# Kernel tuning notes

Hardware: AMD Instinct MI355X
Metric: run time of the kernel (lower is better)

Reference implementation:

```python
import jax, jax.numpy as jnp
import numpy as np

B, S, HID, NH = 4, 2048, 1024, 16
HD = HID // NH  # head_dim = 64


def setup_inputs() -> dict:
    key = jax.random.key(0)
    ks = jax.random.split(key, 5)
    scale = 0.02
    return {
        "hidden_states": jax.random.normal(ks[0], (B, S, HID), dtype=jnp.float32),
        "attention_mask": jnp.zeros((B, 1, 1, S), dtype=jnp.float32),
        "Wq": jax.random.normal(ks[1], (HID, HID), dtype=jnp.float32) * scale,
        "bq": jnp.zeros((HID,), dtype=jnp.float32),
        "Wk": jax.random.normal(ks[2], (HID, HID), dtype=jnp.float32) * scale,
        "bk": jnp.zeros((HID,), dtype=jnp.float32),
        "Wv": jax.random.normal(ks[3], (HID, HID), dtype=jnp.float32) * scale,
        "bv": jnp.zeros((HID,), dtype=jnp.float32),
    }


def _split_heads(x):
    # [B, S, HID] -> [B, NH, S, HD]
    b, s, _ = x.shape
    return x.reshape(b, s, NH, HD).transpose(0, 2, 1, 3)


def reference(hidden_states, attention_mask, Wq, bq, Wk, bk, Wv, bv):
    # Linear projections (torch Linear: x @ W.T + b)
    q = _split_heads(hidden_states @ Wq.T + bq)
    k = _split_heads(hidden_states @ Wk.T + bk)
    v = _split_heads(hidden_states @ Wv.T + bv)

    # scores: [B, NH, S, S]
    scores = jnp.einsum("bhqd,bhkd->bhqk", q, k) / jnp.sqrt(jnp.float32(HD))
    scores = scores + attention_mask  # additive mask, broadcast over heads/query
    weights = jax.nn.softmax(scores, axis=-1)
    # dropout prob = 0 (inference), head_mask = None

    context = jnp.einsum("bhqk,bhkd->bhqd", weights, v)
    # [B, NH, S, HD] -> [B, S, HID]
    context = context.transpose(0, 2, 1, 3).reshape(hidden_states.shape[0], hidden_states.shape[1], HID)
    return context
```

## Files before the change

kernel.cpp:

```cpp
#include <hip/hip_runtime.h>
#include <stdint.h>


typedef float f32x4 __attribute__((ext_vector_type(4)));
typedef float f32x16 __attribute__((ext_vector_type(16)));
typedef __bf16 bf16x8 __attribute__((ext_vector_type(8)));
typedef unsigned short ushort_t;

#define MFMA16(a, b, c) __builtin_amdgcn_mfma_f32_16x16x32_bf16(a, b, c, 0, 0, 0)
#define MFMA32(a, b, c) __builtin_amdgcn_mfma_f32_32x32x16_bf16(a, b, c, 0, 0, 0)

__device__ __forceinline__ ushort_t f2b(float f) {
    union { float f; uint32_t u; } x{f};
    uint32_t r = (x.u + 0x7fffu + ((x.u >> 16) & 1u)) >> 16;
    return (ushort_t)r;
}

__device__ __forceinline__ void gld_lds16(const void* g, void* l) {
    __builtin_amdgcn_global_load_lds(
        (const __attribute__((address_space(1))) unsigned int*)g,
        (__attribute__((address_space(3))) unsigned int*)l, 16, 0, 0);
}

__global__ __launch_bounds__(256) void convert_k(
    const float* __restrict__ hs, const float* __restrict__ wq,
    const float* __restrict__ wk, const float* __restrict__ wv,
    ushort_t* __restrict__ hs_b, ushort_t* __restrict__ w_b) {
    size_t c = (size_t)blockIdx.x * 256 + threadIdx.x;
    size_t i = c * 8;
    const size_t NHS = (size_t)8192 * 1024;
    const float* src;
    ushort_t* dst;
    if (i < NHS) { src = hs + i; dst = hs_b + i; }
    else {
        size_t j = i - NHS;
        int w = (int)(j >> 20);
        size_t o = j & ((1u << 20) - 1);
        src = (w == 0 ? wq : (w == 1 ? wk : wv)) + o;
        dst = w_b + ((size_t)w << 20) + o;
    }
    float4 a = *(const float4*)src;
    float4 b = *(const float4*)(src + 4);
    uint32_t p0 = (uint32_t)f2b(a.x) | ((uint32_t)f2b(a.y) << 16);
    uint32_t p1 = (uint32_t)f2b(a.z) | ((uint32_t)f2b(a.w) << 16);
    uint32_t p2 = (uint32_t)f2b(b.x) | ((uint32_t)f2b(b.y) << 16);
    uint32_t p3 = (uint32_t)f2b(b.z) | ((uint32_t)f2b(b.w) << 16);
    uint4 v{p0, p1, p2, p3};
    *(uint4*)dst = v;
}

__global__ __launch_bounds__(256, 2) void qkv_gemm(
    const ushort_t* __restrict__ Ab, const ushort_t* __restrict__ Wb,
    const float* __restrict__ bq, const float* __restrict__ bk,
    const float* __restrict__ bv, ushort_t* __restrict__ q_ws,
    ushort_t* __restrict__ k_ws, ushort_t* __restrict__ vt_ws) {
    __shared__ __align__(16) char smem_raw[128 * 136 * 2];
    ushort_t* At = (ushort_t*)smem_raw;
    ushort_t* Bt = At + 128 * 64;
    ushort_t* Ct = (ushort_t*)smem_raw;
    int which = blockIdx.z;
    const ushort_t* W = Wb + ((size_t)which << 20);
    int m0 = blockIdx.y * 128, n0 = blockIdx.x * 128;
    int t = threadIdx.x, lane = t & 63, wave = t >> 6;
    int quad = lane >> 4, l16 = lane & 15;
    int wr = (wave >> 1) * 64, wc = (wave & 1) * 64;
    f32x4 acc[4][4] = {};
    for (int k0 = 0; k0 < 1024; k0 += 64) {
        for (int r = 0; r < 4; r++) {
            int idx = r * 256 + t;
            int row = idx >> 3, co = (idx & 7) * 8;
            gld_lds16(Ab + (size_t)(m0 + row) * 1024 + k0 + co, At + idx * 8);
            gld_lds16(W + (size_t)(n0 + row) * 1024 + k0 + co, Bt + idx * 8);
        }
        asm volatile("s_waitcnt vmcnt(0)" ::: "memory");
        __syncthreads();
        for (int kk = 0; kk < 2; kk++) {
            bf16x8 af[4], bf[4];
            for (int i = 0; i < 4; i++)
                af[i] = *(const bf16x8*)(At + (wr + i * 16 + l16) * 64 + kk * 32 + quad * 8);
            for (int j = 0; j < 4; j++)
                bf[j] = *(const bf16x8*)(Bt + (wc + j * 16 + l16) * 64 + kk * 32 + quad * 8);
            for (int i = 0; i < 4; i++)
                for (int j = 0; j < 4; j++)
                    acc[i][j] = MFMA16(af[i], bf[j], acc[i][j]);
        }
        __syncthreads();
    }
    const float* bias = which == 0 ? bq : (which == 1 ? bk : bv);
    float sc = which == 0 ? 0.125f : 1.0f;
    if (which == 2) {
        for (int j = 0; j < 4; j++) {
            float bias_v = bias[n0 + wc + j * 16 + l16];
            for (int i = 0; i < 4; i++) {
                ushort4 pk;
                pk.x = f2b(acc[i][j].x + bias_v);
                pk.y = f2b(acc[i][j].y + bias_v);
                pk.z = f2b(acc[i][j].z + bias_v);
                pk.w = f2b(acc[i][j].w + bias_v);
                *(ushort4*)(Ct + (wc + j * 16 + l16) * 136 + wr + i * 16 + quad * 4) = pk;
            }
        }
    } else {
        for (int j = 0; j < 4; j++) {
            float bias_v = bias[n0 + wc + j * 16 + l16];
            int col = wc + j * 16 + l16;
            for (int i = 0; i < 4; i++) {
                int rb = wr + i * 16 + quad * 4;
                Ct[(rb + 0) * 136 + col] = f2b((acc[i][j].x + bias_v) * sc);
                Ct[(rb + 1) * 136 + col] = f2b((acc[i][j].y + bias_v) * sc);
                Ct[(rb + 2) * 136 + col] = f2b((acc[i][j].z + bias_v) * sc);
                Ct[(rb + 3) * 136 + col] = f2b((acc[i][j].w + bias_v) * sc);
            }
        }
    }
    __syncthreads();
    for (int r = 0; r < 8; r++) {
        int idx = r * 256 + t;
        int row = idx >> 4, c8 = (idx & 15) * 8;
        uint4 val = *(const uint4*)(Ct + row * 136 + c8);
        if (which == 2) {
            int col = n0 + row, h = col >> 6, d = col & 63;
            int tok = m0 + c8, b = tok >> 11, s = tok & 2047;
            *(uint4*)(vt_ws + ((size_t)(b * 16 + h) * 64 + d) * 2048 + s) = val;
        } else {
            int tok = m0 + row, b = tok >> 11, s = tok & 2047;
            int col = n0 + c8, h = col >> 6, d = col & 63;
            ushort_t* base = which == 0 ? q_ws : k_ws;
            *(uint4*)(base + ((size_t)(b * 16 + h) * 2048 + s) * 64 + d) = val;
        }
    }
}

__global__ __launch_bounds__(256, 4) void attn_k(
    const ushort_t* __restrict__ q_ws, const ushort_t* __restrict__ k_ws,
    const ushort_t* __restrict__ vt_ws, const float* __restrict__ mask,
    float* __restrict__ out) {
    __shared__ __align__(16) ushort_t Kl[64 * 72];
    __shared__ __align__(16) ushort_t Vtl[64 * 72];
    __shared__ __align__(16) ushort_t Pl[4][32 * 72];
    int bh = blockIdx.y, b = bh >> 4, h = bh & 15;
    int q0 = blockIdx.x * 128;
    int t = threadIdx.x, lane = t & 63, w = t >> 6;
    int l31 = lane & 31, hi = lane >> 5;
    const ushort_t* Q = q_ws + (size_t)bh * 2048 * 64;
    const ushort_t* K = k_ws + (size_t)bh * 2048 * 64;
    const ushort_t* Vt = vt_ws + (size_t)bh * 64 * 2048;
    const float* mrow = mask + b * 2048;

    bf16x8 qf[4];
#pragma unroll
    for (int c = 0; c < 4; c++)
        qf[c] = *(const bf16x8*)(Q + (size_t)(q0 + w * 32 + l31) * 64 + c * 16 + hi * 8);
    f32x16 o0 = {}, o1 = {};
    float rsum[16];
#pragma unroll
    for (int r = 0; r < 16; r++) rsum[r] = 0.f;

    for (int t0 = 0; t0 < 2048; t0 += 64) {
#pragma unroll
        for (int r = 0; r < 2; r++) {
            int idx = r * 256 + t;
            int row = idx >> 3, co = (idx & 7) * 8;
            *(uint4*)(Kl + row * 72 + co) = *(const uint4*)(K + (size_t)(t0 + row) * 64 + co);
            *(uint4*)(Vtl + row * 72 + co) = *(const uint4*)(Vt + (size_t)row * 2048 + t0 + co);
        }
        float mk0 = mrow[t0 + l31];
        float mk1 = mrow[t0 + 32 + l31];
        __syncthreads();
        f32x16 s0 = {}, s1 = {};
#pragma unroll
        for (int c = 0; c < 4; c++) {
            bf16x8 k0 = *(const bf16x8*)(Kl + l31 * 72 + c * 16 + hi * 8);
            bf16x8 k1 = *(const bf16x8*)(Kl + (32 + l31) * 72 + c * 16 + hi * 8);
            s0 = MFMA32(qf[c], k0, s0);
            s1 = MFMA32(qf[c], k1, s1);
        }
        ushort_t* Pw = Pl[w];
#pragma unroll
        for (int r = 0; r < 16; r++) {
            int prow = (r & 3) + 8 * (r >> 2) + 4 * hi;
            float p0 = __expf(s0[r] + mk0);
            float p1 = __expf(s1[r] + mk1);
            rsum[r] += p0 + p1;
            Pw[prow * 72 + l31] = f2b(p0);
            Pw[prow * 72 + 32 + l31] = f2b(p1);
        }
        asm volatile("s_waitcnt lgkmcnt(0)" ::: "memory");
#pragma unroll
        for (int c = 0; c < 4; c++) {
            bf16x8 pf = *(const bf16x8*)(Pw + l31 * 72 + c * 16 + hi * 8);
            bf16x8 v0 = *(const bf16x8*)(Vtl + l31 * 72 + c * 16 + hi * 8);
            bf16x8 v1 = *(const bf16x8*)(Vtl + (32 + l31) * 72 + c * 16 + hi * 8);
            o0 = MFMA32(pf, v0, o0);
            o1 = MFMA32(pf, v1, o1);
        }
        __syncthreads();
    }
#pragma unroll
    for (int m = 1; m < 32; m <<= 1)
#pragma unroll
        for (int r = 0; r < 16; r++)
            rsum[r] += __shfl_xor(rsum[r], m, 64);
#pragma unroll
    for (int r = 0; r < 16; r++) {
        float inv = 1.f / rsum[r];
        int srow = q0 + w * 32 + (r & 3) + 8 * (r >> 2) + 4 * hi;
        size_t rb = ((size_t)(b * 2048 + srow)) * 1024 + h * 64;
        out[rb + l31] = o0[r] * inv;
        out[rb + 32 + l31] = o1[r] * inv;
    }
}

extern "C" void kernel_launch(void* const* d_in, const int* in_sizes, int n_in,
                              void* d_out, int out_size, void* d_ws, size_t ws_size,
                              hipStream_t stream) {
    const float* hs = (const float*)d_in[0];
    const float* mask = (const float*)d_in[1];
    const float* wq = (const float*)d_in[2];
    const float* bq = (const float*)d_in[3];
    const float* wk = (const float*)d_in[4];
    const float* bk = (const float*)d_in[5];
    const float* wv = (const float*)d_in[6];
    const float* bv = (const float*)d_in[7];
    float* out = (float*)d_out;
    char* ws = (char*)d_ws;
    ushort_t* hs_b = (ushort_t*)ws;
    ushort_t* w_b = (ushort_t*)(ws + 16777216);
    ushort_t* q_ws = (ushort_t*)(ws + 23068672);
    ushort_t* k_ws = (ushort_t*)(ws + 39845888);
    ushort_t* vt_ws = (ushort_t*)(ws + 56623104);

    convert_k<<<5632, 256, 0, stream>>>(hs, wq, wk, wv, hs_b, w_b);
    qkv_gemm<<<dim3(8, 64, 3), 256, 0, stream>>>(hs_b, w_b, bq, bk, bv, q_ws, k_ws, vt_ws);
    attn_k<<<dim3(16, 64), 256, 0, stream>>>(q_ws, k_ws, vt_ws, mask, out);
}
```

Before: 284.1 us.

## Transpose attention MFMAs to keep P in registers, swizzle LDS, use exp2

Rewrites the attention kernel to compute S^T = K·Q^T, so each lane holds probabilities for a single query row. P is then repacked into bf16 fragments with lane shuffles, removing the LDS round trip for P. K and V^T tiles are loaded with direct global-to-LDS loads into an XOR-swizzled layout without padding. Softmax switches to exp2 with log2(e) folded into the Q scale and a pre-scaled mask held in LDS, and the row sum becomes a single scalar per lane. Output goes through an LDS transpose so global stores are coalesced. This adds shuffle and permute work and uses truncating bf16 packing instead of round-to-nearest.

Measured after the change: 266.2 us. 6.3% less time.

```diff
diff --git a/kernel.cpp b/kernel.cpp
--- a/kernel.cpp
+++ b/kernel.cpp
@@ -6,6 +6,7 @@
 typedef float f32x16 __attribute__((ext_vector_type(16)));
 typedef __bf16 bf16x8 __attribute__((ext_vector_type(8)));
 typedef unsigned short ushort_t;
+typedef uint32_t u32;
 
 #define MFMA16(a, b, c) __builtin_amdgcn_mfma_f32_16x16x32_bf16(a, b, c, 0, 0, 0)
 #define MFMA32(a, b, c) __builtin_amdgcn_mfma_f32_32x32x16_bf16(a, b, c, 0, 0, 0)
@@ -14,6 +15,25 @@
     union { float f; uint32_t u; } x{f};
     uint32_t r = (x.u + 0x7fffu + ((x.u >> 16) & 1u)) >> 16;
     return (ushort_t)r;
+}
+
+__device__ __forceinline__ float fexp2(float x) {
+#if __has_builtin(__builtin_amdgcn_exp2f)
+    return __builtin_amdgcn_exp2f(x);
+#else
+    return exp2f(x);
+#endif
+}
+
+__device__ __forceinline__ u32 pkpair(float e, float o) {
+    union { float f; u32 u; } xe{e}, xo{o};
+    return __builtin_amdgcn_perm(xo.u, xe.u, 0x07060302u);
+}
+
+__device__ __forceinline__ bf16x8 mk8(u32 a, u32 b, u32 c, u32 d) {
+    union { u32 u[4]; bf16x8 v; } x;
+    x.u[0] = a; x.u[1] = b; x.u[2] = c; x.u[3] = d;
+    return x.v;
 }
 
 __device__ __forceinline__ void gld_lds16(const void* g, void* l) {
@@ -87,7 +107,7 @@
         __syncthreads();
     }
     const float* bias = which == 0 ? bq : (which == 1 ? bk : bv);
-    float sc = which == 0 ? 0.125f : 1.0f;
+    float sc = which == 0 ? (0.125f * 1.44269504f) : 1.0f;
     if (which == 2) {
         for (int j = 0; j < 4; j++) {
             float bias_v = bias[n0 + wc + j * 16 + l16];
@@ -135,79 +155,118 @@
     const ushort_t* __restrict__ q_ws, const ushort_t* __restrict__ k_ws,
     const ushort_t* __restrict__ vt_ws, const float* __restrict__ mask,
     float* __restrict__ out) {
-    __shared__ __align__(16) ushort_t Kl[64 * 72];
-    __shared__ __align__(16) ushort_t Vtl[64 * 72];
-    __shared__ __align__(16) ushort_t Pl[4][32 * 72];
+    __shared__ __align__(16) char smraw[128 * 65 * 4];
+    ushort_t* Kl = (ushort_t*)smraw;
+    ushort_t* Vtl = Kl + 64 * 64;
+    float* Ml2 = (float*)(smraw + 16384);
+    float* Ot = (float*)smraw;
+
     int bh = blockIdx.y, b = bh >> 4, h = bh & 15;
     int q0 = blockIdx.x * 128;
     int t = threadIdx.x, lane = t & 63, w = t >> 6;
     int l31 = lane & 31, hi = lane >> 5;
+    bool h0 = (hi == 0);
     const ushort_t* Q = q_ws + (size_t)bh * 2048 * 64;
     const ushort_t* K = k_ws + (size_t)bh * 2048 * 64;
     const ushort_t* Vt = vt_ws + (size_t)bh * 64 * 2048;
-    const float* mrow = mask + b * 2048;
-
+
+    for (int r = 0; r < 8; r++) {
+        int i = r * 256 + t;
+        Ml2[i] = mask[b * 2048 + i] * 1.44269504f;
+    }
     bf16x8 qf[4];
 #pragma unroll
-    for (int c = 0; c < 4; c++)
-        qf[c] = *(const bf16x8*)(Q + (size_t)(q0 + w * 32 + l31) * 64 + c * 16 + hi * 8);
+    for (int cs = 0; cs < 4; cs++)
+        qf[cs] = *(const bf16x8*)(Q + (size_t)(q0 + w * 32 + l31) * 64 + cs * 16 + hi * 8);
+    int co[4];
+#pragma unroll
+    for (int cs = 0; cs < 4; cs++)
+        co[cs] = ((cs * 2 + hi) ^ (l31 & 7)) * 8;
+
     f32x16 o0 = {}, o1 = {};
-    float rsum[16];
-#pragma unroll
-    for (int r = 0; r < 16; r++) rsum[r] = 0.f;
+    float rs = 0.f;
 
     for (int t0 = 0; t0 < 2048; t0 += 64) {
 #pragma unroll
-        for (int r = 0; r < 2; r++) {
-            int idx = r * 256 + t;
-            int row = idx >> 3, co = (idx & 7) * 8;
-            *(uint4*)(Kl + row * 72 + co) = *(const uint4*)(K + (size_t)(t0 + row) * 64 + co);
-            *(uint4*)(Vtl + row * 72 + co) = *(const uint4*)(Vt + (size_t)row * 2048 + t0 + co);
-        }
-        float mk0 = mrow[t0 + l31];
-        float mk1 = mrow[t0 + 32 + l31];
+        for (int it = 0; it < 2; it++) {
+            int idx = it * 256 + t;
+            int row = idx >> 3, ch = idx & 7;
+            int sch = (ch ^ (row & 7)) * 8;
+            gld_lds16(K + (size_t)(t0 + row) * 64 + sch, Kl + idx * 8);
+            gld_lds16(Vt + (size_t)row * 2048 + t0 + sch, Vtl + idx * 8);
+        }
+        asm volatile("s_waitcnt vmcnt(0)" ::: "memory");
         __syncthreads();
         f32x16 s0 = {}, s1 = {};
 #pragma unroll
-        for (int c = 0; c < 4; c++) {
-            bf16x8 k0 = *(const bf16x8*)(Kl + l31 * 72 + c * 16 + hi * 8);
-            bf16x8 k1 = *(const bf16x8*)(Kl + (32 + l31) * 72 + c * 16 + hi * 8);
-            s0 = MFMA32(qf[c], k0, s0);
-            s1 = MFMA32(qf[c], k1, s1);
-        }
-        ushort_t* Pw = Pl[w];
-#pragma unroll
-        for (int r = 0; r < 16; r++) {
-            int prow = (r & 3) + 8 * (r >> 2) + 4 * hi;
-            float p0 = __expf(s0[r] + mk0);
-            float p1 = __expf(s1[r] + mk1);
-            rsum[r] += p0 + p1;
-            Pw[prow * 72 + l31] = f2b(p0);
-            Pw[prow * 72 + 32 + l31] = f2b(p1);
-        }
-        asm volatile("s_waitcnt lgkmcnt(0)" ::: "memory");
-#pragma unroll
-        for (int c = 0; c < 4; c++) {
-            bf16x8 pf = *(const bf16x8*)(Pw + l31 * 72 + c * 16 + hi * 8);
-            bf16x8 v0 = *(const bf16x8*)(Vtl + l31 * 72 + c * 16 + hi * 8);
-            bf16x8 v1 = *(const bf16x8*)(Vtl + (32 + l31) * 72 + c * 16 + hi * 8);
-            o0 = MFMA32(pf, v0, o0);
-            o1 = MFMA32(pf, v1, o1);
-        }
-        __syncthreads();
-    }
-#pragma unroll
-    for (int m = 1; m < 32; m <<= 1)
-#pragma unroll
-        for (int r = 0; r < 16; r++)
-            rsum[r] += __shfl_xor(rsum[r], m, 64);
+        for (int cs = 0; cs < 4; cs++) {
+            bf16x8 k0 = *(const bf16x8*)(Kl + l31 * 64 + co[cs]);
+            bf16x8 k1 = *(const bf16x8*)(Kl + (32 + l31) * 64 + co[cs]);
+            s0 = MFMA32(k0, qf[cs], s0);
+            s1 = MFMA32(k1, qf[cs], s1);
+        }
+        u32 pa[8], pb[8];
+#pragma unroll
+        for (int i = 0; i < 4; i++) {
+            f32x4 bm = *(const f32x4*)(Ml2 + t0 + 8 * i + 4 * hi);
+            float e0 = fexp2(s0[4 * i + 0] + bm[0]);
+            float e1 = fexp2(s0[4 * i + 1] + bm[1]);
+            float e2 = fexp2(s0[4 * i + 2] + bm[2]);
+            float e3 = fexp2(s0[4 * i + 3] + bm[3]);
+            rs += (e0 + e1) + (e2 + e3);
+            pa[2 * i] = pkpair(e0, e1);
+            pa[2 * i + 1] = pkpair(e2, e3);
+        }
+#pragma unroll
+        for (int i = 0; i < 4; i++) {
+            f32x4 bm = *(const f32x4*)(Ml2 + t0 + 32 + 8 * i + 4 * hi);
+            float e0 = fexp2(s1[4 * i + 0] + bm[0]);
+            float e1 = fexp2(s1[4 * i + 1] + bm[1]);
+            float e2 = fexp2(s1[4 * i + 2] + bm[2]);
+            float e3 = fexp2(s1[4 * i + 3] + bm[3]);
+            rs += (e0 + e1) + (e2 + e3);
+            pb[2 * i] = pkpair(e0, e1);
+            pb[2 * i + 1] = pkpair(e2, e3);
+        }
+        bf16x8 pfr[4];
+#pragma unroll
+        for (int g = 0; g < 4; g++) {
+            const u32* aa = (g < 2) ? pa : pb;
+            int base = (g & 1) * 4;
+            u32 y0 = h0 ? aa[base + 2] : aa[base + 0];
+            u32 y1 = h0 ? aa[base + 3] : aa[base + 1];
+            u32 sy0 = (u32)__shfl_xor((int)y0, 32, 64);
+            u32 sy1 = (u32)__shfl_xor((int)y1, 32, 64);
+            pfr[g] = mk8(h0 ? aa[base + 0] : sy0, h0 ? aa[base + 1] : sy1,
+                         h0 ? sy0 : aa[base + 2], h0 ? sy1 : aa[base + 3]);
+        }
+#pragma unroll
+        for (int cs = 0; cs < 4; cs++) {
+            bf16x8 v0 = *(const bf16x8*)(Vtl + l31 * 64 + co[cs]);
+            bf16x8 v1 = *(const bf16x8*)(Vtl + (32 + l31) * 64 + co[cs]);
+            o0 = MFMA32(v0, pfr[cs], o0);
+            o1 = MFMA32(v1, pfr[cs], o1);
+        }
+        __syncthreads();
+    }
+    rs += __shfl_xor(rs, 32, 64);
+    float inv = 1.f / rs;
 #pragma unroll
     for (int r = 0; r < 16; r++) {
-        float inv = 1.f / rsum[r];
-        int srow = q0 + w * 32 + (r & 3) + 8 * (r >> 2) + 4 * hi;
-        size_t rb = ((size_t)(b * 2048 + srow)) * 1024 + h * 64;
-        out[rb + l31] = o0[r] * inv;
-        out[rb + 32 + l31] = o1[r] * inv;
+        int d = (r & 3) + 8 * (r >> 2) + 4 * hi;
+        Ot[(w * 32 + l31) * 65 + d] = o0[r] * inv;
+        Ot[(w * 32 + l31) * 65 + 32 + d] = o1[r] * inv;
+    }
+    __syncthreads();
+#pragma unroll
+    for (int p = 0; p < 2; p++) {
+        int row = p * 64 + (t >> 2), colb = (t & 3) * 16;
+        size_t gb = ((size_t)(b * 2048 + q0 + row)) * 1024 + h * 64 + colb;
+#pragma unroll
+        for (int i = 0; i < 4; i++) {
+            f32x4 vv = *(const f32x4*)(Ot + row * 65 + colb + i * 4);
+            *(f32x4*)(out + gb + i * 4) = vv;
+        }
     }
 }
 
```
